# Kernel tuning notes

Measured on AMD Instinct MI355X. Metric: run time of the kernel, lower is better.

The kernel has to match this reference:

```python
import jax, jax.numpy as jnp
import numpy as np

NH = 8  # num_heads


def _conv1x1(w, b, x):
    # 1x1 conv == channel matmul: w [O,C], x [B,C,H,W]
    return jnp.einsum('oc,bchw->bohw', w, x) + b[None, :, None, None]


def _fwd(low_freq_feat, high_freq_feat, ext_context, road_feat,
         ext_proj_w, ext_proj_b, road_proj_w, road_proj_b,
         ext_qkv_w, ext_qkv_b, road_qkv_w, road_qkv_b,
         ext_out_w, ext_out_b, road_out_w, road_out_b,
         gate_ext_w, gate_ext_b, gate_road_w, gate_road_b):
    B, C, H, W = low_freq_feat.shape
    nh = NH
    hd = C // nh
    HW = H * W
    scale = hd ** -0.5

    ext_p = ext_context @ ext_proj_w.T + ext_proj_b          # [B,C]
    road_p = _conv1x1(road_proj_w, road_proj_b, road_feat)   # [B,C,H,W]

    eqkv = (ext_p @ ext_qkv_w.T + ext_qkv_b).reshape(B, 3, nh, hd)
    ext_q, ext_v = eqkv[:, 0], eqkv[:, 2]                    # [B,nh,hd]

    # torch: conv out [B,3C,H,W] viewed as (B,C,3,H,W) -> q/k/v interleaved over channels
    rqkv = _conv1x1(road_qkv_w, road_qkv_b, road_p).reshape(B, C, 3, H, W)
    road_k = rqkv[:, :, 1].reshape(B, nh, hd, HW).transpose(0, 1, 3, 2)  # [B,nh,HW,hd]
    road_v = rqkv[:, :, 2].reshape(B, nh, hd, HW).transpose(0, 1, 3, 2)

    # ext->road attention. The torch code expands ext_q to HW identical rows; one row
    # per (batch, head) gives a bit-identical result without the [B,nh,HW,HW] blowup.
    scores = jnp.einsum('bnd,bnpd->bnp', ext_q, road_k) * scale
    attn = jax.nn.softmax(scores, axis=-1)                   # [B,nh,HW]
    ext_head = jnp.einsum('bnp,bnpd->bnd', attn, road_v).reshape(B, C)
    ext_vec = ext_head @ ext_out_w.T + ext_out_b             # [B,C]
    ext_feat_spatial = jnp.broadcast_to(ext_vec[:, :, None, None], (B, C, H, W))

    # road->ext attention: all HW keys/values are copies of the single ext token, so
    # softmax is exactly uniform and the output per position is exactly ext_v. The
    # road_out 1x1 conv on a spatially-constant map is a single matvec per batch.
    road_vec = ext_v.reshape(B, C) @ road_out_w.T + road_out_b
    road_enhanced = jnp.broadcast_to(road_vec[:, :, None, None], (B, C, H, W))

    # gated fusion (ext stream): spatial mean of constant map == ext_vec
    gate_in = jnp.concatenate([low_freq_feat.mean(axis=(2, 3)), ext_vec], axis=-1)
    ext_gate = jax.nn.sigmoid(gate_in @ gate_ext_w.T + gate_ext_b)[:, :, None, None]
    ext_final = low_freq_feat * (1.0 - ext_gate) + ext_feat_spatial * ext_gate

    # gated fusion (road stream)
    rg_in = jnp.concatenate([high_freq_feat, road_enhanced], axis=1)  # [B,2C,H,W]
    road_gate = jax.nn.sigmoid(_conv1x1(gate_road_w, gate_road_b, rg_in))
    road_final = high_freq_feat * (1.0 - road_gate) + road_enhanced * road_gate
    return ext_final, road_final


def setup_inputs() -> dict:
    key = jax.random.key(0)
    ks = jax.random.split(key, 20)
    B, C, H, W, E = 8, 256, 64, 64, 64
    f = lambda k, shape, s=1.0: jax.random.normal(k, shape, dtype=jnp.float32) * s
    return {
        'low_freq_feat': f(ks[0], (B, C, H, W)),
        'high_freq_feat': f(ks[1], (B, C, H, W)),
        'ext_context': f(ks[2], (B, E)),
        'road_feat': f(ks[3], (B, C, H, W)),
        'ext_proj_w': f(ks[4], (C, E), 0.05), 'ext_proj_b': f(ks[5], (C,), 0.02),
        'road_proj_w': f(ks[6], (C, C), 0.05), 'road_proj_b': f(ks[7], (C,), 0.02),
        'ext_qkv_w': f(ks[8], (3 * C, C), 0.05), 'ext_qkv_b': f(ks[9], (3 * C,), 0.02),
        'road_qkv_w': f(ks[10], (3 * C, C), 0.05), 'road_qkv_b': f(ks[11], (3 * C,), 0.02),
        'ext_out_w': f(ks[12], (C, C), 0.05), 'ext_out_b': f(ks[13], (C,), 0.02),
        'road_out_w': f(ks[14], (C, C), 0.05), 'road_out_b': f(ks[15], (C,), 0.02),
        'gate_ext_w': f(ks[16], (C, 2 * C), 0.05), 'gate_ext_b': f(ks[17], (C,), 0.02),
        'gate_road_w': f(ks[18], (C, 2 * C), 0.05), 'gate_road_b': f(ks[19], (C,), 0.02),
    }


def reference(low_freq_feat, high_freq_feat, ext_context, road_feat,
              ext_proj_w, ext_proj_b, road_proj_w, road_proj_b,
              ext_qkv_w, ext_qkv_b, road_qkv_w, road_qkv_b,
              ext_out_w, ext_out_b, road_out_w, road_out_b,
              gate_ext_w, gate_ext_b, gate_road_w, gate_road_b):
    return _fwd(low_freq_feat, high_freq_feat, ext_context, road_feat,
                ext_proj_w, ext_proj_b, road_proj_w, road_proj_b,
                ext_qkv_w, ext_qkv_b, road_qkv_w, road_qkv_b,
                ext_out_w, ext_out_b, road_out_w, road_out_b,
                gate_ext_w, gate_ext_b, gate_road_w, gate_road_b)
```

## Files before the change

### kernel.cpp

```cpp
#include <hip/hip_runtime.h>

typedef short bf16x8 __attribute__((ext_vector_type(8)));
typedef float f32x4 __attribute__((ext_vector_type(4)));

__device__ __forceinline__ unsigned short f2b(float f) {
    unsigned int u = __builtin_bit_cast(unsigned int, f);
    unsigned int r = u + 0x7FFFu + ((u >> 16) & 1u);
    return (unsigned short)(r >> 16);
}
__device__ __forceinline__ float wsum64(float v) {
    #pragma unroll
    for (int m = 32; m; m >>= 1) v += __shfl_xor(v, m, 64);
    return v;
}

__global__ __launch_bounds__(256) void k_setup(const float* __restrict__ w1,
                                               const float* __restrict__ wqkv,
                                               const float* __restrict__ b1,
                                               const float* __restrict__ bqkv,
                                               const float* __restrict__ gate_road_w,
                                               const float* __restrict__ ext_proj_w,
                                               const float* __restrict__ ext_qkv_w,
                                               const float* __restrict__ road_out_w,
                                               const float* __restrict__ low,
                                               unsigned short* __restrict__ W3b,
                                               unsigned short* __restrict__ Wcb,
                                               unsigned short* __restrict__ WF,
                                               float* __restrict__ bcv,
                                               float* __restrict__ mean_low) {
    int bid = blockIdx.x, t = threadIdx.x;
    __shared__ float sel[8][256];
    __shared__ float red[8][4];
    if (bid >= 400) {
        int bc = bid - 400;
        const f32x4* p4 = (const f32x4*)(low + (size_t)bc * 4096);
        float s = 0.f;
        for (int i = t; i < 1024; i += 256) {
            f32x4 v = p4[i];
            s += v[0] + v[1] + v[2] + v[3];
        }
        s = wsum64(s);
        if ((t & 63) == 0) red[0][t >> 6] = s;
        __syncthreads();
        if (t == 0) mean_low[bc] = (red[0][0] + red[0][1] + red[0][2] + red[0][3]) * (1.0f / 4096.0f);
    } else if (bid < 256) {
        int i = bid * 256 + t;
        int o = i >> 8, k = i & 255;
        W3b[i] = f2b(gate_road_w[o * 512 + k]);
    } else if (bid < 320) {
        int o0 = (bid - 256) * 8;
        #pragma unroll
        for (int r = 0; r < 8; r++) {
            int o = o0 + r;
            int c = (o < 256) ? o : o - 256;
            int g = (o < 256) ? 1 : 2;
            sel[r][t] = wqkv[(size_t)(3 * c + g) * 256 + t];
        }
        __syncthreads();
        float b1v = b1[t];
        #pragma unroll
        for (int r = 0; r < 8; r++) {
            float v = wsum64(sel[r][t] * b1v);
            if ((t & 63) == 0) red[r][t >> 6] = v;
        }
        __syncthreads();
        if (t < 8) {
            int o = o0 + t;
            int c = (o < 256) ? o : o - 256;
            int g = (o < 256) ? 1 : 2;
            bcv[o] = red[t][0] + red[t][1] + red[t][2] + red[t][3] + bqkv[3 * c + g];
        }
        float acc[8] = {};
        #pragma unroll 16
        for (int m = 0; m < 256; m++) {
            float w1v = w1[(size_t)m * 256 + t];
            #pragma unroll
            for (int r = 0; r < 8; r++) acc[r] += sel[r][m] * w1v;
        }
        #pragma unroll
        for (int r = 0; r < 8; r++) Wcb[(size_t)(o0 + r) * 256 + t] = f2b(acc[r]);
    } else {
        int mb = bid - 320;
        int m = mb >> 4, ctile = mb & 15;
        const float* src;
        int stride, K, coff;
        unsigned short* dst;
        if (m == 0)      { src = ext_qkv_w;                    stride = 256; K = 256; coff = 0;   dst = WF; }
        else if (m == 1) { src = ext_qkv_w + (size_t)512 * 256; stride = 256; K = 256; coff = 0;   dst = WF + 65536; }
        else if (m == 2) { src = road_out_w;                   stride = 256; K = 256; coff = 0;   dst = WF + 131072; }
        else if (m == 3) { src = gate_road_w;                  stride = 512; K = 256; coff = 256; dst = WF + 196608; }
        else             { src = ext_proj_w;                   stride = 64;  K = 64;  coff = 0;   dst = WF + 262144; }
        int lc = t >> 4, kseg = t & 15;
        int k0 = kseg * 16;
        if (k0 < K) {
            int c = ctile * 16 + lc;
            const float* sp = src + (size_t)c * stride + coff + k0;
            f32x4 v0 = *(const f32x4*)sp;
            f32x4 v1 = *(const f32x4*)(sp + 4);
            f32x4 v2 = *(const f32x4*)(sp + 8);
            f32x4 v3 = *(const f32x4*)(sp + 12);
            int kk = kseg >> 1;
            int Kt = K >> 5;
            #pragma unroll
            for (int h = 0; h < 2; h++) {
                int lhi = (kseg & 1) * 2 + h;
                int lane = lhi * 16 + lc;
                bf16x8 o;
                f32x4 a = h ? v2 : v0, b = h ? v3 : v1;
                #pragma unroll
                for (int i = 0; i < 4; i++) { o[i] = (short)f2b(a[i]); o[4 + i] = (short)f2b(b[i]); }
                *(bf16x8*)(dst + ((size_t)(ctile * Kt + kk) << 9) + lane * 8) = o;
            }
        }
    }
}

__global__ __launch_bounds__(256) void k_tiny(const unsigned short* __restrict__ WF,
                                              const float* __restrict__ ext_context,
                                              const float* __restrict__ ext_proj_b,
                                              const float* __restrict__ ext_qkv_b,
                                              const float* __restrict__ road_out_b,
                                              const float* __restrict__ gate_road_b,
                                              float* __restrict__ ext_q,
                                              float* __restrict__ road_vec,
                                              float* __restrict__ rg_const) {
    __shared__ unsigned short xA[16][264];
    __shared__ unsigned short xB[16][264];
    int t = threadIdx.x;
    int w = t >> 6, lane = t & 63, l15 = lane & 15, lhi = lane >> 4;
    const unsigned short* WqF  = WF;
    const unsigned short* WvF  = WF + 65536;
    const unsigned short* WroF = WF + 131072;
    const unsigned short* WgF  = WF + 196608;
    const unsigned short* WpF  = WF + 262144;
    for (int i = t; i < 8 * 132; i += 256) {
        int r = 8 + i / 132, cc = (i % 132) * 2;
        *(unsigned int*)&xA[r][cc] = 0;
        *(unsigned int*)&xB[r][cc] = 0;
    }
    {
        int b = t >> 5, k0 = (t & 31) * 2;
        float c0v = ext_context[b * 64 + k0];
        float c1v = ext_context[b * 64 + k0 + 1];
        *(unsigned int*)&xA[b][k0] = (unsigned int)f2b(c0v) | ((unsigned int)f2b(c1v) << 16);
    }
    __syncthreads();
    {
        f32x4 acc[4] = {};
        #pragma unroll
        for (int kk = 0; kk < 2; kk++) {
            bf16x8 a = *(const bf16x8*)&xA[l15][kk * 32 + 8 * lhi];
            #pragma unroll
            for (int ni = 0; ni < 4; ni++) {
                int ct = w * 4 + ni;
                bf16x8 bfr = *(const bf16x8*)(WpF + ((size_t)(ct * 2 + kk) << 9) + lane * 8);
                acc[ni] = __builtin_amdgcn_mfma_f32_16x16x32_bf16(a, bfr, acc[ni], 0, 0, 0);
            }
        }
        if (lhi < 2) {
            #pragma unroll
            for (int ni = 0; ni < 4; ni++) {
                int c = w * 64 + ni * 16 + l15;
                float bp = ext_proj_b[c];
                #pragma unroll
                for (int r = 0; r < 4; r++)
                    xB[4 * lhi + r][c] = f2b(acc[ni][r] + bp);
            }
        }
    }
    __syncthreads();
    {
        f32x4 acc[8] = {};
        bool isq = (w < 2);
        int cbase = (w & 1) * 128;
        const unsigned short* Wb = isq ? WqF : WvF;
        for (int kk = 0; kk < 8; kk++) {
            bf16x8 a = *(const bf16x8*)&xB[l15][kk * 32 + 8 * lhi];
            #pragma unroll
            for (int ni = 0; ni < 8; ni++) {
                int ct = (cbase >> 4) + ni;
                bf16x8 bfr = *(const bf16x8*)(Wb + ((size_t)(ct * 8 + kk) << 9) + lane * 8);
                acc[ni] = __builtin_amdgcn_mfma_f32_16x16x32_bf16(a, bfr, acc[ni], 0, 0, 0);
            }
        }
        if (lhi < 2) {
            #pragma unroll
            for (int ni = 0; ni < 8; ni++) {
                int c = cbase + ni * 16 + l15;
                float bb = ext_qkv_b[(isq ? 0 : 512) + c];
                #pragma unroll
                for (int r = 0; r < 4; r++) {
                    int b = 4 * lhi + r;
                    float val = acc[ni][r] + bb;
                    if (isq) ext_q[b * 256 + c] = val;
                    else     xA[b][c] = f2b(val);
                }
            }
        }
    }
    __syncthreads();
    {
        f32x4 acc[4] = {};
        for (int kk = 0; kk < 8; kk++) {
            bf16x8 a = *(const bf16x8*)&xA[l15][kk * 32 + 8 * lhi];
            #pragma unroll
            for (int ni = 0; ni < 4; ni++) {
                int ct = w * 4 + ni;
                bf16x8 bfr = *(const bf16x8*)(WroF + ((size_t)(ct * 8 + kk) << 9) + lane * 8);
                acc[ni] = __builtin_amdgcn_mfma_f32_16x16x32_bf16(a, bfr, acc[ni], 0, 0, 0);
            }
        }
        if (lhi < 2) {
            #pragma unroll
            for (int ni = 0; ni < 4; ni++) {
                int c = w * 64 + ni * 16 + l15;
                float bb = road_out_b[c];
                #pragma unroll
                for (int r = 0; r < 4; r++) {
                    int b = 4 * lhi + r;
                    float val = acc[ni][r] + bb;
                    road_vec[b * 256 + c] = val;
                    xB[b][c] = f2b(val);
                }
            }
        }
    }
    __syncthreads();
    {
        f32x4 acc[4] = {};
        for (int kk = 0; kk < 8; kk++) {
            bf16x8 a = *(const bf16x8*)&xB[l15][kk * 32 + 8 * lhi];
            #pragma unroll
            for (int ni = 0; ni < 4; ni++) {
                int ct = w * 4 + ni;
                bf16x8 bfr = *(const bf16x8*)(WgF + ((size_t)(ct * 8 + kk) << 9) + lane * 8);
                acc[ni] = __builtin_amdgcn_mfma_f32_16x16x32_bf16(a, bfr, acc[ni], 0, 0, 0);
            }
        }
        if (lhi < 2) {
            #pragma unroll
            for (int ni = 0; ni < 4; ni++) {
                int c = w * 64 + ni * 16 + l15;
                float bb = gate_road_b[c];
                #pragma unroll
                for (int r = 0; r < 4; r++)
                    rg_const[(4 * lhi + r) * 256 + c] = acc[ni][r] + bb;
            }
        }
    }
}

__global__ __launch_bounds__(512) void k_kv(const float* __restrict__ road_feat,
                                            const unsigned short* __restrict__ Wcb,
                                            const float* __restrict__ bcv,
                                            const float* __restrict__ extq,
                                            float* __restrict__ part) {
    __shared__ unsigned short Xs[32 * 256];
    __shared__ float esh[8][32];
    char* Xc = (char*)Xs;
    int bid = blockIdx.x;
    int b  = bid >> 7;
    int p0 = (bid & 127) << 5;
    int t  = threadIdx.x;
    const float* rfb = road_feat + (size_t)b * 1048576;

    int c0 = 2 * (t >> 3);
    int j4 = (t & 7) * 4;
    #pragma unroll
    for (int it = 0; it < 2; ++it) {
        int c = c0 + 128 * it;
        f32x4 g0 = *(const f32x4*)(rfb + (size_t)c * 4096 + p0 + j4);
        f32x4 g1 = *(const f32x4*)(rfb + (size_t)(c + 1) * 4096 + p0 + j4);
        #pragma unroll
        for (int i = 0; i < 4; i++) {
            int j = j4 + i;
            unsigned int pk = (unsigned int)f2b(g0[i]) | ((unsigned int)f2b(g1[i]) << 16);
            *(unsigned int*)(Xc + ((j * 512 + 2 * c) ^ ((j & 15) << 4))) = pk;
        }
    }
    __syncthreads();

    int w = t >> 6, lane = t & 63, l15 = lane & 15, lhi = lane >> 4;

    f32x4 acc[2][4] = {};
    for (int kk = 0; kk < 8; kk++) {
        bf16x8 a[2];
        #pragma unroll
        for (int mi = 0; mi < 2; mi++) {
            int j = mi * 16 + l15;
            int off = (j * 512 + (kk * 32 + 8 * lhi) * 2) ^ ((j & 15) << 4);
            a[mi] = *(const bf16x8*)((const char*)Xs + off);
        }
        #pragma unroll
        for (int ni = 0; ni < 4; ni++) {
            int n = w * 64 + ni * 16 + l15;
            bf16x8 bf = *(const bf16x8*)(Wcb + (size_t)n * 256 + kk * 32 + 8 * lhi);
            acc[0][ni] = __builtin_amdgcn_mfma_f32_16x16x32_bf16(a[0], bf, acc[0][ni], 0, 0, 0);
            acc[1][ni] = __builtin_amdgcn_mfma_f32_16x16x32_bf16(a[1], bf, acc[1][ni], 0, 0, 0);
        }
    }

    if (w < 4) {
        float qv[4], bk[4];
        #pragma unroll
        for (int ni = 0; ni < 4; ni++) {
            int n = w * 64 + ni * 16 + l15;
            qv[ni] = extq[b * 256 + n];
            bk[ni] = bcv[n];
        }
        #pragma unroll
        for (int mi = 0; mi < 2; mi++)
            #pragma unroll
            for (int r = 0; r < 4; r++) {
                int j = mi * 16 + 4 * lhi + r;
                #pragma unroll
                for (int hl = 0; hl < 2; hl++) {
                    float s = (acc[mi][2 * hl][r] + bk[2 * hl]) * qv[2 * hl]
                            + (acc[mi][2 * hl + 1][r] + bk[2 * hl + 1]) * qv[2 * hl + 1];
                    s += __shfl_xor(s, 1, 64);
                    s += __shfl_xor(s, 2, 64);
                    s += __shfl_xor(s, 4, 64);
                    s += __shfl_xor(s, 8, 64);
                    if (l15 == 0)
                        esh[w * 2 + hl][j] = expf(s * 0.17677669529663687f);
                }
            }
    }
    __syncthreads();

    float* pb = part + (size_t)bid * 264;
    if (w >= 4) {
        #pragma unroll
        for (int ni = 0; ni < 4; ni++) {
            int cv = (w - 4) * 64 + ni * 16 + l15;
            int hg = (w - 4) * 2 + (ni >> 1);
            float bv = bcv[256 + cv];
            float p = 0.f;
            #pragma unroll
            for (int mi = 0; mi < 2; mi++)
                #pragma unroll
                for (int r = 0; r < 4; r++) {
                    int j = mi * 16 + 4 * lhi + r;
                    p += esh[hg][j] * (acc[mi][ni][r] + bv);
                }
            p += __shfl_xor(p, 16, 64);
            p += __shfl_xor(p, 32, 64);
            if (lhi == 0) pb[8 + cv] = p;
        }
    } else {
        int h0 = w * 2;
        float v0 = (lane < 32) ? esh[h0][lane] : esh[h0 + 1][lane - 32];
        v0 += __shfl_xor(v0, 1, 64);
        v0 += __shfl_xor(v0, 2, 64);
        v0 += __shfl_xor(v0, 4, 64);
        v0 += __shfl_xor(v0, 8, 64);
        v0 += __shfl_xor(v0, 16, 64);
        if (lane == 0)  pb[h0] = v0;
        if (lane == 32) pb[h0 + 1] = v0;
    }
}

__global__ __launch_bounds__(256) void k_vec(const float* __restrict__ part,
                                             const float* __restrict__ ext_out_w,
                                             const float* __restrict__ ext_out_b,
                                             const float* __restrict__ mean_low,
                                             const float* __restrict__ gate_ext_w,
                                             const float* __restrict__ gate_ext_b,
                                             float* __restrict__ ext_vec,
                                             float* __restrict__ ext_gate) {
    int b = blockIdx.x, c = threadIdx.x;
    __shared__ float hd_[256], ev[256], ml[256], tot[8];
    const float* pb = part + (size_t)b * 128 * 264;
    float a = 0.f;
    #pragma unroll 4
    for (int tile = 0; tile < 128; tile++) a += pb[tile * 264 + 8 + c];
    if (c < 8) {
        float s = 0.f;
        for (int tile = 0; tile < 128; tile++) s += pb[tile * 264 + c];
        tot[c] = 1.0f / s;
    }
    ml[c] = mean_low[b * 256 + c];
    __syncthreads();
    hd_[c] = a * tot[c >> 5];
    __syncthreads();
    float s = ext_out_b[c];
    #pragma unroll 4
    for (int k = 0; k < 256; k++) s += ext_out_w[c * 256 + k] * hd_[k];
    ext_vec[b * 256 + c] = s;
    ev[c] = s;
    __syncthreads();
    float z = gate_ext_b[c];
    #pragma unroll 4
    for (int k = 0; k < 256; k++)
        z += gate_ext_w[c * 512 + k] * ml[k] + gate_ext_w[c * 512 + 256 + k] * ev[k];
    ext_gate[b * 256 + c] = 1.0f / (1.0f + expf(-z));
}

__global__ __launch_bounds__(256) void k_ext_final(const float* __restrict__ low,
                                                   const float* __restrict__ ext_vec,
                                                   const float* __restrict__ ext_gate,
                                                   float* __restrict__ out) {
    int idx = blockIdx.x * 256 + threadIdx.x;
    #pragma unroll
    for (int rep = 0; rep < 4; ++rep) {
        int i = idx + rep * 524288;
        int bc = i >> 10;
        float g = ext_gate[bc];
        float vv = ext_vec[bc];
        f32x4 L = *(const f32x4*)(low + (size_t)i * 4);
        f32x4 o;
        #pragma unroll
        for (int c = 0; c < 4; c++) o[c] = L[c] + g * (vv - L[c]);
        *(f32x4*)(out + (size_t)i * 4) = o;
    }
}

__global__ __launch_bounds__(512) void k_road(const float* __restrict__ high,
                                              const unsigned short* __restrict__ W3b,
                                              const float* __restrict__ rg_const,
                                              const float* __restrict__ road_vec,
                                              float* __restrict__ outbuf) {
    __shared__ float Xs[32 * 256];
    char* Xc = (char*)Xs;
    int bid = blockIdx.x;
    int b  = bid >> 7;
    int p0 = (bid & 127) << 5;
    int t  = threadIdx.x;
    const float* hb = high + (size_t)b * 1048576;

    int c0 = t >> 3;
    int j4 = (t & 7) * 4;
    #pragma unroll
    for (int it = 0; it < 4; ++it) {
        int c = c0 + 64 * it;
        f32x4 g = *(const f32x4*)(hb + (size_t)c * 4096 + p0 + j4);
        #pragma unroll
        for (int i = 0; i < 4; i++) {
            int j = j4 + i;
            *(float*)(Xc + ((j * 1024 + 4 * c) ^ ((j & 15) << 4))) = g[i];
        }
    }
    __syncthreads();

    int w = t >> 6, lane = t & 63, l15 = lane & 15, lhi = lane >> 4;
    f32x4 acc[2][2] = {};
    for (int kk = 0; kk < 8; kk++) {
        bf16x8 a[2];
        #pragma unroll
        for (int mi = 0; mi < 2; mi++) {
            int j = mi * 16 + l15;
            int base = j * 1024 + (kk * 32 + 8 * lhi) * 4;
            int sw = (j & 15) << 4;
            f32x4 x0 = *(const f32x4*)(Xc + (base ^ sw));
            f32x4 x1 = *(const f32x4*)(Xc + ((base + 16) ^ sw));
            bf16x8 av;
            #pragma unroll
            for (int i = 0; i < 4; i++) {
                av[i]     = (short)f2b(x0[i]);
                av[4 + i] = (short)f2b(x1[i]);
            }
            a[mi] = av;
        }
        #pragma unroll
        for (int ni = 0; ni < 2; ni++) {
            int o = w * 32 + ni * 16 + l15;
            bf16x8 bf = *(const bf16x8*)(W3b + (size_t)o * 256 + kk * 32 + 8 * lhi);
            acc[0][ni] = __builtin_amdgcn_mfma_f32_16x16x32_bf16(a[0], bf, acc[0][ni], 0, 0, 0);
            acc[1][ni] = __builtin_amdgcn_mfma_f32_16x16x32_bf16(a[1], bf, acc[1][ni], 0, 0, 0);
        }
    }
    __syncthreads();

    #pragma unroll
    for (int ni = 0; ni < 2; ni++) {
        int o = w * 32 + ni * 16 + l15;
        float rc = rg_const[b * 256 + o];
        float rv = road_vec[b * 256 + o];
        #pragma unroll
        for (int mi = 0; mi < 2; mi++)
            #pragma unroll
            for (int r = 0; r < 4; r++) {
                int j = mi * 16 + 4 * lhi + r;
                float* slot = (float*)(Xc + ((j * 1024 + 4 * o) ^ ((j & 15) << 4)));
                float z = acc[mi][ni][r] + rc;
                float gte = 1.0f / (1.0f + expf(-z));
                float hv = *slot;
                *slot = hv + gte * (rv - hv);
            }
    }
    __syncthreads();

    float* ob = outbuf + 8388608 + (size_t)b * 1048576;
    #pragma unroll
    for (int it = 0; it < 4; ++it) {
        int c = c0 + 64 * it;
        f32x4 o4;
        #pragma unroll
        for (int i = 0; i < 4; i++) {
            int j = j4 + i;
            o4[i] = *(const float*)(Xc + ((j * 1024 + 4 * c) ^ ((j & 15) << 4)));
        }
        *(f32x4*)(ob + (size_t)c * 4096 + p0 + j4) = o4;
    }
}

extern "C" void kernel_launch(void* const* d_in, const int* in_sizes, int n_in,
                              void* d_out, int out_size, void* d_ws, size_t ws_size,
                              hipStream_t stream) {
    const float* low         = (const float*)d_in[0];
    const float* high        = (const float*)d_in[1];
    const float* ext_context = (const float*)d_in[2];
    const float* road_feat   = (const float*)d_in[3];
    const float* ext_proj_w  = (const float*)d_in[4];
    const float* ext_proj_b  = (const float*)d_in[5];
    const float* road_proj_w = (const float*)d_in[6];
    const float* road_proj_b = (const float*)d_in[7];
    const float* ext_qkv_w   = (const float*)d_in[8];
    const float* ext_qkv_b   = (const float*)d_in[9];
    const float* road_qkv_w  = (const float*)d_in[10];
    const float* road_qkv_b  = (const float*)d_in[11];
    const float* ext_out_w   = (const float*)d_in[12];
    const float* ext_out_b   = (const float*)d_in[13];
    const float* road_out_w  = (const float*)d_in[14];
    const float* road_out_b  = (const float*)d_in[15];
    const float* gate_ext_w  = (const float*)d_in[16];
    const float* gate_ext_b  = (const float*)d_in[17];
    const float* gate_road_w = (const float*)d_in[18];
    const float* gate_road_b = (const float*)d_in[19];

    float* out = (float*)d_out;
    unsigned short* wsb = (unsigned short*)d_ws;
    unsigned short* Wcb = wsb;
    unsigned short* W3b = wsb + 131072;
    unsigned short* WF  = wsb + 196608;
    float* fw = (float*)((char*)d_ws + 983040);
    float* ext_q    = fw;
    float* road_vec = fw + 2048;
    float* rg_const = fw + 4096;
    float* ext_vec  = fw + 8192;
    float* ext_gate = fw + 10240;
    float* mean_low = fw + 12288;
    float* bcv      = fw + 14336;
    float* part = out + 2097152;

    k_setup<<<2448, 256, 0, stream>>>(road_proj_w, road_qkv_w, road_proj_b, road_qkv_b,
                                      gate_road_w, ext_proj_w, ext_qkv_w, road_out_w, low,
                                      W3b, Wcb, WF, bcv, mean_low);
    k_tiny<<<1, 256, 0, stream>>>(WF, ext_context, ext_proj_b, ext_qkv_b,
                                  road_out_b, gate_road_b, ext_q, road_vec, rg_const);
    k_kv<<<1024, 512, 0, stream>>>(road_feat, Wcb, bcv, ext_q, part);
    k_vec<<<8, 256, 0, stream>>>(part, ext_out_w, ext_out_b, mean_low,
                                 gate_ext_w, gate_ext_b, ext_vec, ext_gate);
    k_ext_final<<<2048, 256, 0, stream>>>(low, ext_vec, ext_gate, out);
    k_road<<<1024, 512, 0, stream>>>(high, W3b, rg_const, road_vec, out);
}
```

Baseline: 171.3 us.

## Merge road-gate kernel into KV kernel via block-role split

Fuses the independent k_kv and k_road kernels into one k_main launch, where even blocks do the K/V attention-partial work and odd blocks do the road gated-fusion work. Both roles share one 33 KB shared-memory buffer. The K loops are also restructured so each wave preloads all eight weight fragments per output tile before issuing the MFMAs. The goal is to save a kernel launch and let the memory-bound road work overlap with the KV work on the GPU. The cost is a larger shared allocation for the KV role and more register pressure from the preloaded fragments, which could lower occupancy.

```diff
diff --git a/kernel.cpp b/kernel.cpp
--- a/kernel.cpp
+++ b/kernel.cpp
@@ -85,11 +85,11 @@
         const float* src;
         int stride, K, coff;
         unsigned short* dst;
-        if (m == 0)      { src = ext_qkv_w;                    stride = 256; K = 256; coff = 0;   dst = WF; }
+        if (m == 0)      { src = ext_qkv_w;                     stride = 256; K = 256; coff = 0;   dst = WF; }
         else if (m == 1) { src = ext_qkv_w + (size_t)512 * 256; stride = 256; K = 256; coff = 0;   dst = WF + 65536; }
-        else if (m == 2) { src = road_out_w;                   stride = 256; K = 256; coff = 0;   dst = WF + 131072; }
-        else if (m == 3) { src = gate_road_w;                  stride = 512; K = 256; coff = 256; dst = WF + 196608; }
-        else             { src = ext_proj_w;                   stride = 64;  K = 64;  coff = 0;   dst = WF + 262144; }
+        else if (m == 2) { src = road_out_w;                    stride = 256; K = 256; coff = 0;   dst = WF + 131072; }
+        else if (m == 3) { src = gate_road_w;                   stride = 512; K = 256; coff = 256; dst = WF + 196608; }
+        else             { src = ext_proj_w;                    stride = 64;  K = 64;  coff = 0;   dst = WF + 262144; }
         int lc = t >> 4, kseg = t & 15;
         int k0 = kseg * 16;
         if (k0 < K) {
@@ -250,113 +250,194 @@
     }
 }
 
-__global__ __launch_bounds__(512) void k_kv(const float* __restrict__ road_feat,
-                                            const unsigned short* __restrict__ Wcb,
-                                            const float* __restrict__ bcv,
-                                            const float* __restrict__ extq,
-                                            float* __restrict__ part) {
-    __shared__ unsigned short Xs[32 * 256];
-    __shared__ float esh[8][32];
-    char* Xc = (char*)Xs;
+__global__ __launch_bounds__(512) void k_main(const float* __restrict__ road_feat,
+                                              const float* __restrict__ high,
+                                              const unsigned short* __restrict__ Wcb,
+                                              const unsigned short* __restrict__ W3b,
+                                              const float* __restrict__ bcv,
+                                              const float* __restrict__ extq,
+                                              const float* __restrict__ rg_const,
+                                              const float* __restrict__ road_vec,
+                                              float* __restrict__ part,
+                                              float* __restrict__ outbuf) {
+    __shared__ __align__(16) char smem[33792];
     int bid = blockIdx.x;
-    int b  = bid >> 7;
-    int p0 = (bid & 127) << 5;
+    int role = bid & 1, tile = bid >> 1;
+    int b  = tile >> 7;
+    int p0 = (tile & 127) << 5;
     int t  = threadIdx.x;
-    const float* rfb = road_feat + (size_t)b * 1048576;
-
-    int c0 = 2 * (t >> 3);
-    int j4 = (t & 7) * 4;
-    #pragma unroll
-    for (int it = 0; it < 2; ++it) {
-        int c = c0 + 128 * it;
-        f32x4 g0 = *(const f32x4*)(rfb + (size_t)c * 4096 + p0 + j4);
-        f32x4 g1 = *(const f32x4*)(rfb + (size_t)(c + 1) * 4096 + p0 + j4);
-        #pragma unroll
-        for (int i = 0; i < 4; i++) {
-            int j = j4 + i;
-            unsigned int pk = (unsigned int)f2b(g0[i]) | ((unsigned int)f2b(g1[i]) << 16);
-            *(unsigned int*)(Xc + ((j * 512 + 2 * c) ^ ((j & 15) << 4))) = pk;
-        }
-    }
-    __syncthreads();
-
     int w = t >> 6, lane = t & 63, l15 = lane & 15, lhi = lane >> 4;
 
-    f32x4 acc[2][4] = {};
-    for (int kk = 0; kk < 8; kk++) {
-        bf16x8 a[2];
-        #pragma unroll
-        for (int mi = 0; mi < 2; mi++) {
-            int j = mi * 16 + l15;
-            int off = (j * 512 + (kk * 32 + 8 * lhi) * 2) ^ ((j & 15) << 4);
-            a[mi] = *(const bf16x8*)((const char*)Xs + off);
-        }
+    if (role == 0) {
+        char* Xc = smem;
+        float (*esh)[32] = (float (*)[32])(smem + 16384);
+        const float* rfb = road_feat + (size_t)b * 1048576;
+        int c0 = 2 * (t >> 3);
+        int j4 = (t & 7) * 4;
+        #pragma unroll
+        for (int it = 0; it < 2; ++it) {
+            int c = c0 + 128 * it;
+            f32x4 g0 = *(const f32x4*)(rfb + (size_t)c * 4096 + p0 + j4);
+            f32x4 g1 = *(const f32x4*)(rfb + (size_t)(c + 1) * 4096 + p0 + j4);
+            #pragma unroll
+            for (int i = 0; i < 4; i++) {
+                int j = j4 + i;
+                unsigned int pk = (unsigned int)f2b(g0[i]) | ((unsigned int)f2b(g1[i]) << 16);
+                *(unsigned int*)(Xc + ((j * 512 + 2 * c) ^ ((j & 15) << 4))) = pk;
+            }
+        }
+        __syncthreads();
+
+        f32x4 acc[2][4] = {};
         #pragma unroll
         for (int ni = 0; ni < 4; ni++) {
-            int n = w * 64 + ni * 16 + l15;
-            bf16x8 bf = *(const bf16x8*)(Wcb + (size_t)n * 256 + kk * 32 + 8 * lhi);
-            acc[0][ni] = __builtin_amdgcn_mfma_f32_16x16x32_bf16(a[0], bf, acc[0][ni], 0, 0, 0);
-            acc[1][ni] = __builtin_amdgcn_mfma_f32_16x16x32_bf16(a[1], bf, acc[1][ni], 0, 0, 0);
-        }
-    }
-
-    if (w < 4) {
-        float qv[4], bk[4];
-        #pragma unroll
-        for (int ni = 0; ni < 4; ni++) {
-            int n = w * 64 + ni * 16 + l15;
-            qv[ni] = extq[b * 256 + n];
-            bk[ni] = bcv[n];
-        }
-        #pragma unroll
-        for (int mi = 0; mi < 2; mi++)
-            #pragma unroll
-            for (int r = 0; r < 4; r++) {
-                int j = mi * 16 + 4 * lhi + r;
-                #pragma unroll
-                for (int hl = 0; hl < 2; hl++) {
-                    float s = (acc[mi][2 * hl][r] + bk[2 * hl]) * qv[2 * hl]
-                            + (acc[mi][2 * hl + 1][r] + bk[2 * hl + 1]) * qv[2 * hl + 1];
-                    s += __shfl_xor(s, 1, 64);
-                    s += __shfl_xor(s, 2, 64);
-                    s += __shfl_xor(s, 4, 64);
-                    s += __shfl_xor(s, 8, 64);
-                    if (l15 == 0)
-                        esh[w * 2 + hl][j] = expf(s * 0.17677669529663687f);
-                }
-            }
-    }
-    __syncthreads();
-
-    float* pb = part + (size_t)bid * 264;
-    if (w >= 4) {
-        #pragma unroll
-        for (int ni = 0; ni < 4; ni++) {
-            int cv = (w - 4) * 64 + ni * 16 + l15;
-            int hg = (w - 4) * 2 + (ni >> 1);
-            float bv = bcv[256 + cv];
-            float p = 0.f;
+            const unsigned short* wrow = Wcb + (size_t)(w * 64 + ni * 16 + l15) * 256 + 8 * lhi;
+            bf16x8 wf[8];
+            #pragma unroll
+            for (int kk = 0; kk < 8; kk++) wf[kk] = *(const bf16x8*)(wrow + kk * 32);
+            #pragma unroll
+            for (int kk = 0; kk < 8; kk++) {
+                int base = (kk * 32 + 8 * lhi) * 2;
+                bf16x8 a0 = *(const bf16x8*)(Xc + ((l15 * 512 + base) ^ (l15 << 4)));
+                bf16x8 a1 = *(const bf16x8*)(Xc + (((16 + l15) * 512 + base) ^ (l15 << 4)));
+                acc[0][ni] = __builtin_amdgcn_mfma_f32_16x16x32_bf16(a0, wf[kk], acc[0][ni], 0, 0, 0);
+                acc[1][ni] = __builtin_amdgcn_mfma_f32_16x16x32_bf16(a1, wf[kk], acc[1][ni], 0, 0, 0);
+            }
+        }
+
+        if (w < 4) {
+            float qv[4], bk[4];
+            #pragma unroll
+            for (int ni = 0; ni < 4; ni++) {
+                int n = w * 64 + ni * 16 + l15;
+                qv[ni] = extq[b * 256 + n];
+                bk[ni] = bcv[n];
+            }
             #pragma unroll
             for (int mi = 0; mi < 2; mi++)
                 #pragma unroll
                 for (int r = 0; r < 4; r++) {
                     int j = mi * 16 + 4 * lhi + r;
-                    p += esh[hg][j] * (acc[mi][ni][r] + bv);
+                    #pragma unroll
+                    for (int hl = 0; hl < 2; hl++) {
+                        float s = (acc[mi][2 * hl][r] + bk[2 * hl]) * qv[2 * hl]
+                                + (acc[mi][2 * hl + 1][r] + bk[2 * hl + 1]) * qv[2 * hl + 1];
+                        s += __shfl_xor(s, 1, 64);
+                        s += __shfl_xor(s, 2, 64);
+                        s += __shfl_xor(s, 4, 64);
+                        s += __shfl_xor(s, 8, 64);
+                        if (l15 == 0)
+                            esh[w * 2 + hl][j] = expf(s * 0.17677669529663687f);
+                    }
                 }
-            p += __shfl_xor(p, 16, 64);
-            p += __shfl_xor(p, 32, 64);
-            if (lhi == 0) pb[8 + cv] = p;
+        }
+        __syncthreads();
+
+        float* pb = part + (size_t)tile * 264;
+        if (w >= 4) {
+            #pragma unroll
+            for (int ni = 0; ni < 4; ni++) {
+                int cv = (w - 4) * 64 + ni * 16 + l15;
+                int hg = (w - 4) * 2 + (ni >> 1);
+                float bv = bcv[256 + cv];
+                float p = 0.f;
+                #pragma unroll
+                for (int mi = 0; mi < 2; mi++)
+                    #pragma unroll
+                    for (int r = 0; r < 4; r++) {
+                        int j = mi * 16 + 4 * lhi + r;
+                        p += esh[hg][j] * (acc[mi][ni][r] + bv);
+                    }
+                p += __shfl_xor(p, 16, 64);
+                p += __shfl_xor(p, 32, 64);
+                if (lhi == 0) pb[8 + cv] = p;
+            }
+        } else {
+            int h0 = w * 2;
+            float v0 = (lane < 32) ? esh[h0][lane] : esh[h0 + 1][lane - 32];
+            v0 += __shfl_xor(v0, 1, 64);
+            v0 += __shfl_xor(v0, 2, 64);
+            v0 += __shfl_xor(v0, 4, 64);
+            v0 += __shfl_xor(v0, 8, 64);
+            v0 += __shfl_xor(v0, 16, 64);
+            if (lane == 0)  pb[h0] = v0;
+            if (lane == 32) pb[h0 + 1] = v0;
         }
     } else {
-        int h0 = w * 2;
-        float v0 = (lane < 32) ? esh[h0][lane] : esh[h0 + 1][lane - 32];
-        v0 += __shfl_xor(v0, 1, 64);
-        v0 += __shfl_xor(v0, 2, 64);
-        v0 += __shfl_xor(v0, 4, 64);
-        v0 += __shfl_xor(v0, 8, 64);
-        v0 += __shfl_xor(v0, 16, 64);
-        if (lane == 0)  pb[h0] = v0;
-        if (lane == 32) pb[h0 + 1] = v0;
+        char* Xc = smem;
+        const float* hb = high + (size_t)b * 1048576;
+        int c0 = t >> 3;
+        int j4 = (t & 7) * 4;
+        #pragma unroll
+        for (int it = 0; it < 4; ++it) {
+            int c = c0 + 64 * it;
+            f32x4 g = *(const f32x4*)(hb + (size_t)c * 4096 + p0 + j4);
+            #pragma unroll
+            for (int i = 0; i < 4; i++) {
+                int j = j4 + i;
+                *(float*)(Xc + ((j * 1024 + 4 * c) ^ ((j & 15) << 4))) = g[i];
+            }
+        }
+        __syncthreads();
+
+        f32x4 acc[2][2] = {};
+        #pragma unroll
+        for (int ni = 0; ni < 2; ni++) {
+            const unsigned short* wrow = W3b + (size_t)(w * 32 + ni * 16 + l15) * 256 + 8 * lhi;
+            bf16x8 wf[8];
+            #pragma unroll
+            for (int kk = 0; kk < 8; kk++) wf[kk] = *(const bf16x8*)(wrow + kk * 32);
+            #pragma unroll
+            for (int kk = 0; kk < 8; kk++) {
+                int base = (kk * 32 + 8 * lhi) * 4;
+                int sw0 = l15 << 4;
+                f32x4 x0 = *(const f32x4*)(Xc + ((l15 * 1024 + base) ^ sw0));
+                f32x4 x1 = *(const f32x4*)(Xc + ((l15 * 1024 + base + 16) ^ sw0));
+                f32x4 y0 = *(const f32x4*)(Xc + (((16 + l15) * 1024 + base) ^ sw0));
+                f32x4 y1 = *(const f32x4*)(Xc + (((16 + l15) * 1024 + base + 16) ^ sw0));
+                bf16x8 a0, a1;
+                #pragma unroll
+                for (int i = 0; i < 4; i++) {
+                    a0[i] = (short)f2b(x0[i]); a0[4 + i] = (short)f2b(x1[i]);
+                    a1[i] = (short)f2b(y0[i]); a1[4 + i] = (short)f2b(y1[i]);
+                }
+                acc[0][ni] = __builtin_amdgcn_mfma_f32_16x16x32_bf16(a0, wf[kk], acc[0][ni], 0, 0, 0);
+                acc[1][ni] = __builtin_amdgcn_mfma_f32_16x16x32_bf16(a1, wf[kk], acc[1][ni], 0, 0, 0);
+            }
+        }
+        __syncthreads();
+
+        #pragma unroll
+        for (int ni = 0; ni < 2; ni++) {
+            int o = w * 32 + ni * 16 + l15;
+            float rc = rg_const[b * 256 + o];
+            float rv = road_vec[b * 256 + o];
+            #pragma unroll
+            for (int mi = 0; mi < 2; mi++)
+                #pragma unroll
+                for (int r = 0; r < 4; r++) {
+                    int j = mi * 16 + 4 * lhi + r;
+                    float* slot = (float*)(Xc + ((j * 1024 + 4 * o) ^ ((j & 15) << 4)));
+                    float z = acc[mi][ni][r] + rc;
+                    float gte = 1.0f / (1.0f + expf(-z));
+                    float hv = *slot;
+                    *slot = hv + gte * (rv - hv);
+                }
+        }
+        __syncthreads();
+
+        float* ob = outbuf + 8388608 + (size_t)b * 1048576;
+        #pragma unroll
+        for (int it = 0; it < 4; ++it) {
+            int c = c0 + 64 * it;
+            f32x4 o4;
+            #pragma unroll
+            for (int i = 0; i < 4; i++) {
+                int j = j4 + i;
+                o4[i] = *(const float*)(Xc + ((j * 1024 + 4 * c) ^ ((j & 15) << 4)));
+            }
+            *(f32x4*)(ob + (size_t)c * 4096 + p0 + j4) = o4;
+        }
     }
 }
 
@@ -412,95 +493,6 @@
         #pragma unroll
         for (int c = 0; c < 4; c++) o[c] = L[c] + g * (vv - L[c]);
         *(f32x4*)(out + (size_t)i * 4) = o;
-    }
-}
-
-__global__ __launch_bounds__(512) void k_road(const float* __restrict__ high,
-                                              const unsigned short* __restrict__ W3b,
-                                              const float* __restrict__ rg_const,
-                                              const float* __restrict__ road_vec,
-                                              float* __restrict__ outbuf) {
-    __shared__ float Xs[32 * 256];
-    char* Xc = (char*)Xs;
-    int bid = blockIdx.x;
-    int b  = bid >> 7;
-    int p0 = (bid & 127) << 5;
-    int t  = threadIdx.x;
-    const float* hb = high + (size_t)b * 1048576;
-
-    int c0 = t >> 3;
-    int j4 = (t & 7) * 4;
-    #pragma unroll
-    for (int it = 0; it < 4; ++it) {
-        int c = c0 + 64 * it;
-        f32x4 g = *(const f32x4*)(hb + (size_t)c * 4096 + p0 + j4);
-        #pragma unroll
-        for (int i = 0; i < 4; i++) {
-            int j = j4 + i;
-            *(float*)(Xc + ((j * 1024 + 4 * c) ^ ((j & 15) << 4))) = g[i];
-        }
-    }
-    __syncthreads();
-
-    int w = t >> 6, lane = t & 63, l15 = lane & 15, lhi = lane >> 4;
-    f32x4 acc[2][2] = {};
-    for (int kk = 0; kk < 8; kk++) {
-        bf16x8 a[2];
-        #pragma unroll
-        for (int mi = 0; mi < 2; mi++) {
-            int j = mi * 16 + l15;
-            int base = j * 1024 + (kk * 32 + 8 * lhi) * 4;
-            int sw = (j & 15) << 4;
-            f32x4 x0 = *(const f32x4*)(Xc + (base ^ sw));
-            f32x4 x1 = *(const f32x4*)(Xc + ((base + 16) ^ sw));
-            bf16x8 av;
-            #pragma unroll
-            for (int i = 0; i < 4; i++) {
-                av[i]     = (short)f2b(x0[i]);
-                av[4 + i] = (short)f2b(x1[i]);
-            }
-            a[mi] = av;
-        }
-        #pragma unroll
-        for (int ni = 0; ni < 2; ni++) {
-            int o = w * 32 + ni * 16 + l15;
-            bf16x8 bf = *(const bf16x8*)(W3b + (size_t)o * 256 + kk * 32 + 8 * lhi);
-            acc[0][ni] = __builtin_amdgcn_mfma_f32_16x16x32_bf16(a[0], bf, acc[0][ni], 0, 0, 0);
-            acc[1][ni] = __builtin_amdgcn_mfma_f32_16x16x32_bf16(a[1], bf, acc[1][ni], 0, 0, 0);
-        }
-    }
-    __syncthreads();
-
-    #pragma unroll
-    for (int ni = 0; ni < 2; ni++) {
-        int o = w * 32 + ni * 16 + l15;
-        float rc = rg_const[b * 256 + o];
-        float rv = road_vec[b * 256 + o];
-        #pragma unroll
-        for (int mi = 0; mi < 2; mi++)
-            #pragma unroll
-            for (int r = 0; r < 4; r++) {
-                int j = mi * 16 + 4 * lhi + r;
-                float* slot = (float*)(Xc + ((j * 1024 + 4 * o) ^ ((j & 15) << 4)));
-                float z = acc[mi][ni][r] + rc;
-                float gte = 1.0f / (1.0f + expf(-z));
-                float hv = *slot;
-                *slot = hv + gte * (rv - hv);
-            }
-    }
-    __syncthreads();
-
-    float* ob = outbuf + 8388608 + (size_t)b * 1048576;
-    #pragma unroll
-    for (int it = 0; it < 4; ++it) {
-        int c = c0 + 64 * it;
-        f32x4 o4;
-        #pragma unroll
-        for (int i = 0; i < 4; i++) {
-            int j = j4 + i;
-            o4[i] = *(const float*)(Xc + ((j * 1024 + 4 * c) ^ ((j & 15) << 4)));
-        }
-        *(f32x4*)(ob + (size_t)c * 4096 + p0 + j4) = o4;
     }
 }
 
@@ -548,9 +540,9 @@
                                       W3b, Wcb, WF, bcv, mean_low);
     k_tiny<<<1, 256, 0, stream>>>(WF, ext_context, ext_proj_b, ext_qkv_b,
                                   road_out_b, gate_road_b, ext_q, road_vec, rg_const);
-    k_kv<<<1024, 512, 0, stream>>>(road_feat, Wcb, bcv, ext_q, part);
+    k_main<<<2048, 512, 0, stream>>>(road_feat, high, Wcb, W3b, bcv, ext_q,
+                                     rg_const, road_vec, part, out);
     k_vec<<<8, 256, 0, stream>>>(part, ext_out_w, ext_out_b, mean_low,
                                  gate_ext_w, gate_ext_b, ext_vec, ext_gate);
     k_ext_final<<<2048, 256, 0, stream>>>(low, ext_vec, ext_gate, out);
-    k_road<<<1024, 512, 0, stream>>>(high, W3b, rg_const, road_vec, out);
-}
+}
```

Result: slower. 182.1 us (+6.3%).

## Move ext_vec and gate matvecs to MFMA with pre-converted bf16 weights

Applied to the files above, without the earlier changes.

The old k_vec kernel did the ext_out and gate_ext matvecs in fp32 scalar loops, with each of its 8 blocks re-reading the full weight matrices. It is replaced by two kernels. k_vec_combine reduces the attention partials into head outputs, and a single-block k_vec2 runs both matvecs with bf16 MFMA, using weights that k_setup now pre-converts into fragment layout. k_kv and k_road also swizzle block indices so consecutive blocks interleave across batches, and the redundant zeroing of unused LDS rows in k_tiny is dropped. In exchange there is an extra launch and bf16 rounding in those matvecs, and the WF scratch now lives inside the output buffer until k_ext_final overwrites it.

```diff
diff --git a/kernel.cpp b/kernel.cpp
--- a/kernel.cpp
+++ b/kernel.cpp
@@ -13,6 +13,7 @@
     for (int m = 32; m; m >>= 1) v += __shfl_xor(v, m, 64);
     return v;
 }
+
 
 __global__ __launch_bounds__(256) void k_setup(const float* __restrict__ w1,
                                                const float* __restrict__ wqkv,
@@ -22,6 +23,8 @@
                                                const float* __restrict__ ext_proj_w,
                                                const float* __restrict__ ext_qkv_w,
                                                const float* __restrict__ road_out_w,
+                                               const float* __restrict__ ext_out_w,
+                                               const float* __restrict__ gate_ext_w,
                                                const float* __restrict__ low,
                                                unsigned short* __restrict__ W3b,
                                                unsigned short* __restrict__ Wcb,
@@ -31,8 +34,8 @@
     int bid = blockIdx.x, t = threadIdx.x;
     __shared__ float sel[8][256];
     __shared__ float red[8][4];
-    if (bid >= 400) {
-        int bc = bid - 400;
+    if (bid >= 448) {
+        int bc = bid - 448;
         const f32x4* p4 = (const f32x4*)(low + (size_t)bc * 4096);
         float s = 0.f;
         for (int i = t; i < 1024; i += 256) {
@@ -85,11 +88,16 @@
         const float* src;
         int stride, K, coff;
         unsigned short* dst;
-        if (m == 0)      { src = ext_qkv_w;                    stride = 256; K = 256; coff = 0;   dst = WF; }
-        else if (m == 1) { src = ext_qkv_w + (size_t)512 * 256; stride = 256; K = 256; coff = 0;   dst = WF + 65536; }
-        else if (m == 2) { src = road_out_w;                   stride = 256; K = 256; coff = 0;   dst = WF + 131072; }
-        else if (m == 3) { src = gate_road_w;                  stride = 512; K = 256; coff = 256; dst = WF + 196608; }
-        else             { src = ext_proj_w;                   stride = 64;  K = 64;  coff = 0;   dst = WF + 262144; }
+        switch (m) {
+        case 0: src = ext_qkv_w;                     stride = 256; K = 256; coff = 0;   dst = WF;          break;
+        case 1: src = ext_qkv_w + (size_t)512 * 256; stride = 256; K = 256; coff = 0;   dst = WF + 65536;  break;
+        case 2: src = road_out_w;                    stride = 256; K = 256; coff = 0;   dst = WF + 131072; break;
+        case 3: src = gate_road_w;                   stride = 512; K = 256; coff = 256; dst = WF + 196608; break;
+        case 4: src = ext_proj_w;                    stride = 64;  K = 64;  coff = 0;   dst = WF + 262144; break;
+        case 5: src = ext_out_w;                     stride = 256; K = 256; coff = 0;   dst = WF + 278528; break;
+        case 6: src = gate_ext_w;                    stride = 512; K = 256; coff = 0;   dst = WF + 344064; break;
+        default: src = gate_ext_w;                   stride = 512; K = 256; coff = 256; dst = WF + 409600; break;
+        }
         int lc = t >> 4, kseg = t & 15;
         int k0 = kseg * 16;
         if (k0 < K) {
@@ -133,11 +141,6 @@
     const unsigned short* WroF = WF + 131072;
     const unsigned short* WgF  = WF + 196608;
     const unsigned short* WpF  = WF + 262144;
-    for (int i = t; i < 8 * 132; i += 256) {
-        int r = 8 + i / 132, cc = (i % 132) * 2;
-        *(unsigned int*)&xA[r][cc] = 0;
-        *(unsigned int*)&xB[r][cc] = 0;
-    }
     {
         int b = t >> 5, k0 = (t & 31) * 2;
         float c0v = ext_context[b * 64 + k0];
@@ -258,7 +261,7 @@
     __shared__ unsigned short Xs[32 * 256];
     __shared__ float esh[8][32];
     char* Xc = (char*)Xs;
-    int bid = blockIdx.x;
+    int bid = ((blockIdx.x & 7) << 7) | (blockIdx.x >> 3);
     int b  = bid >> 7;
     int p0 = (bid & 127) << 5;
     int t  = threadIdx.x;
@@ -360,40 +363,111 @@
     }
 }
 
-__global__ __launch_bounds__(256) void k_vec(const float* __restrict__ part,
-                                             const float* __restrict__ ext_out_w,
-                                             const float* __restrict__ ext_out_b,
-                                             const float* __restrict__ mean_low,
-                                             const float* __restrict__ gate_ext_w,
-                                             const float* __restrict__ gate_ext_b,
-                                             float* __restrict__ ext_vec,
-                                             float* __restrict__ ext_gate) {
+__global__ __launch_bounds__(256) void k_vec_combine(const float* __restrict__ part,
+                                                     float* __restrict__ hdg) {
     int b = blockIdx.x, c = threadIdx.x;
-    __shared__ float hd_[256], ev[256], ml[256], tot[8];
+    __shared__ float tot[8];
     const float* pb = part + (size_t)b * 128 * 264;
     float a = 0.f;
-    #pragma unroll 4
+    #pragma unroll 8
     for (int tile = 0; tile < 128; tile++) a += pb[tile * 264 + 8 + c];
     if (c < 8) {
         float s = 0.f;
+        #pragma unroll 8
         for (int tile = 0; tile < 128; tile++) s += pb[tile * 264 + c];
         tot[c] = 1.0f / s;
     }
-    ml[c] = mean_low[b * 256 + c];
-    __syncthreads();
-    hd_[c] = a * tot[c >> 5];
-    __syncthreads();
-    float s = ext_out_b[c];
-    #pragma unroll 4
-    for (int k = 0; k < 256; k++) s += ext_out_w[c * 256 + k] * hd_[k];
-    ext_vec[b * 256 + c] = s;
-    ev[c] = s;
-    __syncthreads();
-    float z = gate_ext_b[c];
-    #pragma unroll 4
-    for (int k = 0; k < 256; k++)
-        z += gate_ext_w[c * 512 + k] * ml[k] + gate_ext_w[c * 512 + 256 + k] * ev[k];
-    ext_gate[b * 256 + c] = 1.0f / (1.0f + expf(-z));
+    __syncthreads();
+    hdg[b * 256 + c] = a * tot[c >> 5];
+}
+
+__global__ __launch_bounds__(256) void k_vec2(const unsigned short* __restrict__ WF,
+                                              const float* __restrict__ hdg,
+                                              const float* __restrict__ mean_low,
+                                              const float* __restrict__ ext_out_b,
+                                              const float* __restrict__ gate_ext_b,
+                                              float* __restrict__ ext_vec,
+                                              float* __restrict__ ext_gate) {
+    __shared__ unsigned short xA[16][264];
+    __shared__ unsigned short xB[16][264];
+    __shared__ unsigned short xC[16][264];
+    int t = threadIdx.x;
+    int w = t >> 6, lane = t & 63, l15 = lane & 15, lhi = lane >> 4;
+    const unsigned short* WoF    = WF + 278528;
+    const unsigned short* WgeLoF = WF + 344064;
+    const unsigned short* WgeHiF = WF + 409600;
+    {
+        int bb = t >> 5, kb = t & 31;
+        #pragma unroll
+        for (int q = 0; q < 4; q++) {
+            int k0 = (kb + 32 * q) * 2;
+            *(unsigned int*)&xA[bb][k0] =
+                (unsigned int)f2b(hdg[bb * 256 + k0]) | ((unsigned int)f2b(hdg[bb * 256 + k0 + 1]) << 16);
+            *(unsigned int*)&xB[bb][k0] =
+                (unsigned int)f2b(mean_low[bb * 256 + k0]) | ((unsigned int)f2b(mean_low[bb * 256 + k0 + 1]) << 16);
+        }
+    }
+    __syncthreads();
+    {
+        f32x4 acc[4] = {};
+        for (int kk = 0; kk < 8; kk++) {
+            bf16x8 a = *(const bf16x8*)&xA[l15][kk * 32 + 8 * lhi];
+            #pragma unroll
+            for (int ni = 0; ni < 4; ni++) {
+                int ct = w * 4 + ni;
+                bf16x8 bfr = *(const bf16x8*)(WoF + ((size_t)(ct * 8 + kk) << 9) + lane * 8);
+                acc[ni] = __builtin_amdgcn_mfma_f32_16x16x32_bf16(a, bfr, acc[ni], 0, 0, 0);
+            }
+        }
+        if (lhi < 2) {
+            #pragma unroll
+            for (int ni = 0; ni < 4; ni++) {
+                int c = w * 64 + ni * 16 + l15;
+                float bb = ext_out_b[c];
+                #pragma unroll
+                for (int r = 0; r < 4; r++) {
+                    int b = 4 * lhi + r;
+                    float val = acc[ni][r] + bb;
+                    ext_vec[b * 256 + c] = val;
+                    xC[b][c] = f2b(val);
+                }
+            }
+        }
+    }
+    __syncthreads();
+    {
+        f32x4 acc[4] = {};
+        for (int kk = 0; kk < 8; kk++) {
+            bf16x8 a = *(const bf16x8*)&xB[l15][kk * 32 + 8 * lhi];
+            #pragma unroll
+            for (int ni = 0; ni < 4; ni++) {
+                int ct = w * 4 + ni;
+                bf16x8 bfr = *(const bf16x8*)(WgeLoF + ((size_t)(ct * 8 + kk) << 9) + lane * 8);
+                acc[ni] = __builtin_amdgcn_mfma_f32_16x16x32_bf16(a, bfr, acc[ni], 0, 0, 0);
+            }
+        }
+        for (int kk = 0; kk < 8; kk++) {
+            bf16x8 a = *(const bf16x8*)&xC[l15][kk * 32 + 8 * lhi];
+            #pragma unroll
+            for (int ni = 0; ni < 4; ni++) {
+                int ct = w * 4 + ni;
+                bf16x8 bfr = *(const bf16x8*)(WgeHiF + ((size_t)(ct * 8 + kk) << 9) + lane * 8);
+                acc[ni] = __builtin_amdgcn_mfma_f32_16x16x32_bf16(a, bfr, acc[ni], 0, 0, 0);
+            }
+        }
+        if (lhi < 2) {
+            #pragma unroll
+            for (int ni = 0; ni < 4; ni++) {
+                int c = w * 64 + ni * 16 + l15;
+                float bb = gate_ext_b[c];
+                #pragma unroll
+                for (int r = 0; r < 4; r++) {
+                    int b = 4 * lhi + r;
+                    ext_gate[b * 256 + c] = 1.0f / (1.0f + expf(-(acc[ni][r] + bb)));
+                }
+            }
+        }
+    }
 }
 
 __global__ __launch_bounds__(256) void k_ext_final(const float* __restrict__ low,
@@ -422,7 +496,7 @@
                                               float* __restrict__ outbuf) {
     __shared__ float Xs[32 * 256];
     char* Xc = (char*)Xs;
-    int bid = blockIdx.x;
+    int bid = ((blockIdx.x & 7) << 7) | (blockIdx.x >> 3);
     int b  = bid >> 7;
     int p0 = (bid & 127) << 5;
     int t  = threadIdx.x;
@@ -532,7 +606,6 @@
     unsigned short* wsb = (unsigned short*)d_ws;
     unsigned short* Wcb = wsb;
     unsigned short* W3b = wsb + 131072;
-    unsigned short* WF  = wsb + 196608;
     float* fw = (float*)((char*)d_ws + 983040);
     float* ext_q    = fw;
     float* road_vec = fw + 2048;
@@ -541,16 +614,20 @@
     float* ext_gate = fw + 10240;
     float* mean_low = fw + 12288;
     float* bcv      = fw + 14336;
+    float* hdg      = fw + 16384;
     float* part = out + 2097152;
-
-    k_setup<<<2448, 256, 0, stream>>>(road_proj_w, road_qkv_w, road_proj_b, road_qkv_b,
-                                      gate_road_w, ext_proj_w, ext_qkv_w, road_out_w, low,
+    unsigned short* WF = (unsigned short*)(out + 4194304);
+
+    k_setup<<<2496, 256, 0, stream>>>(road_proj_w, road_qkv_w, road_proj_b, road_qkv_b,
+                                      gate_road_w, ext_proj_w, ext_qkv_w, road_out_w,
+                                      ext_out_w, gate_ext_w, low,
                                       W3b, Wcb, WF, bcv, mean_low);
     k_tiny<<<1, 256, 0, stream>>>(WF, ext_context, ext_proj_b, ext_qkv_b,
                                   road_out_b, gate_road_b, ext_q, road_vec, rg_const);
     k_kv<<<1024, 512, 0, stream>>>(road_feat, Wcb, bcv, ext_q, part);
-    k_vec<<<8, 256, 0, stream>>>(part, ext_out_w, ext_out_b, mean_low,
-                                 gate_ext_w, gate_ext_b, ext_vec, ext_gate);
+    k_vec_combine<<<8, 256, 0, stream>>>(part, hdg);
+    k_vec2<<<1, 256, 0, stream>>>(WF, hdg, mean_low, ext_out_b, gate_ext_b,
+                                  ext_vec, ext_gate);
     k_ext_final<<<2048, 256, 0, stream>>>(low, ext_vec, ext_gate, out);
     k_road<<<1024, 512, 0, stream>>>(high, W3b, rg_const, road_vec, out);
 }
```

Measured after the change: 156.1 us. -8.9%, faster.
